# Kernel tuning notes

Measured on AMD Instinct MI355X. Metric: run time of the kernel, lower is better.

The kernel has to match this reference:

```python
import jax, jax.numpy as jnp
import numpy as np

D_MODEL = 1024
NUM_HEADS = 16
D_K = D_MODEL // NUM_HEADS


def setup_inputs() -> dict:
    key = jax.random.key(0)
    ks = jax.random.split(key, 8)
    B, S = 2, 2048
    query = jax.random.normal(ks[0], (B, S, D_MODEL), dtype=jnp.float32)
    k_in = jax.random.normal(ks[1], (B, S, D_MODEL), dtype=jnp.float32)
    value = jax.random.normal(ks[2], (B, S, D_MODEL), dtype=jnp.float32)
    # causal mask: True = masked out (upper triangle above diagonal)
    mask = jnp.triu(jnp.ones((S, S), dtype=bool), k=1)[None, None, :, :]
    scale = 1.0 / np.sqrt(D_MODEL)
    W_q = jax.random.normal(ks[3], (D_MODEL, D_MODEL), dtype=jnp.float32) * scale
    W_k = jax.random.normal(ks[4], (D_MODEL, D_MODEL), dtype=jnp.float32) * scale
    W_v = jax.random.normal(ks[5], (D_MODEL, D_MODEL), dtype=jnp.float32) * scale
    W_o = jax.random.normal(ks[6], (D_MODEL, D_MODEL), dtype=jnp.float32) * scale
    return {"query": query, "key": k_in, "value": value, "mask": mask,
            "W_q": W_q, "W_k": W_k, "W_v": W_v, "W_o": W_o}


def _split(x):
    # [B, S, d_model] -> [B, h, S, d_k]
    B, S, _ = x.shape
    return x.reshape(B, S, NUM_HEADS, D_K).transpose(0, 2, 1, 3)


def reference(query, key, value, mask, W_q, W_k, W_v, W_o):
    # torch nn.Linear(bias=False): y = x @ W.T
    Q = _split(query @ W_q.T)   # [B, h, Sq, d_k]
    K = _split(key @ W_k.T)     # [B, h, Sk, d_k]
    V = _split(value @ W_v.T)   # [B, h, Sk, d_k]
    scores = jnp.einsum('bhqd,bhkd->bhqk', Q, K) / jnp.sqrt(jnp.float32(D_K))
    scores = jnp.where(mask, -jnp.inf, scores)
    attn_w = jax.nn.softmax(scores, axis=-1)
    attn_w = jnp.nan_to_num(attn_w, nan=0.0)
    out = jnp.einsum('bhqk,bhkd->bhqd', attn_w, V)  # [B, h, Sq, d_k]
    B, _, Sq, _ = out.shape
    merged = out.transpose(0, 2, 1, 3).reshape(B, Sq, D_MODEL)
    return merged @ W_o.T
```

## Files before the change

### kernel.cpp

```cpp
#include <hip/hip_runtime.h>
#include <hip/hip_bf16.h>
#include <stdint.h>

typedef __attribute__((ext_vector_type(4))) float f32x4;
typedef __attribute__((ext_vector_type(8))) __bf16 bf16x8;
typedef __attribute__((ext_vector_type(4))) unsigned short us4;
typedef __attribute__((ext_vector_type(4))) short v4ss;

#define SEQ 2048
#define DMODEL 1024
#define NH 16
#define DK 64
#define MTOT 4096

__device__ __forceinline__ unsigned short f2bf(float x) {
  union { float f; unsigned int u; } v; v.f = x;
  unsigned int r = v.u + 0x7fffu + ((v.u >> 16) & 1u);
  return (unsigned short)(r >> 16);
}

__device__ __forceinline__ f32x4 mfma_bf16(bf16x8 a, bf16x8 b, f32x4 c) {
  return __builtin_amdgcn_mfma_f32_16x16x32_bf16(a, b, c, 0, 0, 0);
}

__device__ __forceinline__ f32x4 mfma_k16(us4 a, us4 b, f32x4 c) {
#if __has_builtin(__builtin_amdgcn_mfma_f32_16x16x16bf16_1k)
  return __builtin_amdgcn_mfma_f32_16x16x16bf16_1k(
      __builtin_bit_cast(v4ss, a), __builtin_bit_cast(v4ss, b), c, 0, 0, 0);
#else
  union U { bf16x8 v; us4 h[2]; } ua, ub;
  us4 z = {0, 0, 0, 0};
  ua.h[0] = a; ua.h[1] = z;
  ub.h[0] = b; ub.h[1] = z;
  return mfma_bf16(ua.v, ub.v, c);
#endif
}

__device__ __forceinline__ void gload16(const unsigned short* g, unsigned short* l) {
  __builtin_amdgcn_global_load_lds((__attribute__((address_space(1))) void*)g,
                                   (__attribute__((address_space(3))) void*)l,
                                   16, 0, 0);
}

__global__ void cvt_all(const float* __restrict__ s0, const float* __restrict__ s1,
                        const float* __restrict__ s2, const float* __restrict__ s3,
                        const float* __restrict__ s4, const float* __restrict__ s5,
                        const float* __restrict__ s6,
                        unsigned short* __restrict__ d0, unsigned short* __restrict__ d1,
                        unsigned short* __restrict__ d2, unsigned short* __restrict__ d3,
                        unsigned short* __restrict__ d4, unsigned short* __restrict__ d5,
                        unsigned short* __restrict__ d6) {
  const int y = blockIdx.y;
  const float* s = y == 0 ? s0 : y == 1 ? s1 : y == 2 ? s2 : y == 3 ? s3
                 : y == 4 ? s4 : y == 5 ? s5 : s6;
  unsigned short* d = y == 0 ? d0 : y == 1 ? d1 : y == 2 ? d2 : y == 3 ? d3
                    : y == 4 ? d4 : y == 5 ? d5 : d6;
  const int n4 = (y < 3) ? (MTOT * DMODEL / 4) : (DMODEL * DMODEL / 4);
  const int stride = gridDim.x * blockDim.x;
  for (int i = blockIdx.x * blockDim.x + threadIdx.x; i < n4; i += stride) {
    f32x4 v = reinterpret_cast<const f32x4*>(s)[i];
    us4 o;
    o.x = f2bf(v.x); o.y = f2bf(v.y); o.z = f2bf(v.z); o.w = f2bf(v.w);
    reinterpret_cast<us4*>(d)[i] = o;
  }
}

__global__ __launch_bounds__(256) void gemm_qkv(
    const unsigned short* __restrict__ xq, const unsigned short* __restrict__ xk,
    const unsigned short* __restrict__ xv, const unsigned short* __restrict__ bwq,
    const unsigned short* __restrict__ bwk, const unsigned short* __restrict__ bwv,
    unsigned short* __restrict__ Qh, unsigned short* __restrict__ Kh,
    unsigned short* __restrict__ Vt) {
  const int z = blockIdx.z;
  const unsigned short* A = z == 0 ? xq : (z == 1 ? xk : xv);
  const unsigned short* B = z == 0 ? bwq : (z == 1 ? bwk : bwv);
  unsigned short* out = z == 0 ? Qh : (z == 1 ? Kh : Vt);
  const float scale = z == 0 ? 0.18033688011112042f : 1.0f;

  __shared__ __align__(16) unsigned short lA[128 * 32];
  __shared__ __align__(16) unsigned short lB[128 * 32];
  const int tid = threadIdx.x;
  const int lane = tid & 63;
  const int wid = tid >> 6;
  const int l15 = lane & 15, l4 = lane >> 4;
  const int bm = blockIdx.x, bn = blockIdx.y;
  const int wr = wid >> 1, wc = wid & 1;

  f32x4 acc[4][4] = {};

  const int chunk0 = (wid * 2 + 0) * 64 + lane;
  const int chunk1 = (wid * 2 + 1) * 64 + lane;
  const unsigned short* gA0 = A + (size_t)(bm * 128 + (chunk0 >> 2)) * 1024 + (chunk0 & 3) * 8;
  const unsigned short* gA1 = A + (size_t)(bm * 128 + (chunk1 >> 2)) * 1024 + (chunk1 & 3) * 8;
  const unsigned short* gB0 = B + (size_t)(bn * 128 + (chunk0 >> 2)) * 1024 + (chunk0 & 3) * 8;
  const unsigned short* gB1 = B + (size_t)(bn * 128 + (chunk1 >> 2)) * 1024 + (chunk1 & 3) * 8;
  unsigned short* lA0 = lA + (wid * 2 + 0) * 512;
  unsigned short* lA1 = lA + (wid * 2 + 1) * 512;
  unsigned short* lB0 = lB + (wid * 2 + 0) * 512;
  unsigned short* lB1 = lB + (wid * 2 + 1) * 512;

  for (int kt = 0; kt < 1024; kt += 32) {
    __syncthreads();
    gload16(gA0 + kt, lA0);
    gload16(gA1 + kt, lA1);
    gload16(gB0 + kt, lB0);
    gload16(gB1 + kt, lB1);
    __syncthreads();
    bf16x8 af[4], bfr[4];
#pragma unroll
    for (int i = 0; i < 4; ++i)
      af[i] = *reinterpret_cast<const bf16x8*>(&lA[(wr * 64 + i * 16 + l15) * 32 + l4 * 8]);
#pragma unroll
    for (int j = 0; j < 4; ++j)
      bfr[j] = *reinterpret_cast<const bf16x8*>(&lB[(wc * 64 + j * 16 + l15) * 32 + l4 * 8]);
#pragma unroll
    for (int i = 0; i < 4; ++i)
#pragma unroll
      for (int j = 0; j < 4; ++j)
        acc[i][j] = mfma_bf16(af[i], bfr[j], acc[i][j]);
  }

  const int row0 = bm * 128 + wr * 64;
  const int col0 = bn * 128 + wc * 64;

  if (z < 2) {
#pragma unroll
    for (int i = 0; i < 4; ++i) {
#pragma unroll
      for (int j = 0; j < 4; ++j) {
        const int n = col0 + j * 16 + l15;
        const int h = n >> 6, dd = n & 63;
#pragma unroll
        for (int r = 0; r < 4; ++r) {
          const int m = row0 + i * 16 + l4 * 4 + r;
          const int b = m >> 11, s = m & 2047;
          out[(size_t)(b * NH + h) * (SEQ * DK) + s * DK + dd] = f2bf(acc[i][j][r] * scale);
        }
      }
    }
  } else {
#pragma unroll
    for (int i = 0; i < 4; ++i) {
      const int m0 = row0 + i * 16 + l4 * 4;
      const int b = m0 >> 11, s0 = m0 & 2047;
#pragma unroll
      for (int j = 0; j < 4; ++j) {
        const int n = col0 + j * 16 + l15;
        const int h = n >> 6, dd = n & 63;
        us4 pk;
        pk.x = f2bf(acc[i][j][0]);
        pk.y = f2bf(acc[i][j][1]);
        pk.z = f2bf(acc[i][j][2]);
        pk.w = f2bf(acc[i][j][3]);
        *reinterpret_cast<us4*>(&out[(size_t)(b * NH + h) * (DK * SEQ) + dd * SEQ + s0]) = pk;
      }
    }
  }
}

__global__ __launch_bounds__(256) void gemm_o(const unsigned short* __restrict__ A,
                                              const unsigned short* __restrict__ B,
                                              float* __restrict__ out) {
  __shared__ __align__(16) unsigned short lA[128 * 32];
  __shared__ __align__(16) unsigned short lB[128 * 32];
  const int tid = threadIdx.x;
  const int lane = tid & 63;
  const int wid = tid >> 6;
  const int l15 = lane & 15, l4 = lane >> 4;
  const int bm = blockIdx.x, bn = blockIdx.y;
  const int wr = wid >> 1, wc = wid & 1;

  f32x4 acc[4][4] = {};

  const int chunk0 = (wid * 2 + 0) * 64 + lane;
  const int chunk1 = (wid * 2 + 1) * 64 + lane;
  const unsigned short* gA0 = A + (size_t)(bm * 128 + (chunk0 >> 2)) * 1024 + (chunk0 & 3) * 8;
  const unsigned short* gA1 = A + (size_t)(bm * 128 + (chunk1 >> 2)) * 1024 + (chunk1 & 3) * 8;
  const unsigned short* gB0 = B + (size_t)(bn * 128 + (chunk0 >> 2)) * 1024 + (chunk0 & 3) * 8;
  const unsigned short* gB1 = B + (size_t)(bn * 128 + (chunk1 >> 2)) * 1024 + (chunk1 & 3) * 8;
  unsigned short* lA0 = lA + (wid * 2 + 0) * 512;
  unsigned short* lA1 = lA + (wid * 2 + 1) * 512;
  unsigned short* lB0 = lB + (wid * 2 + 0) * 512;
  unsigned short* lB1 = lB + (wid * 2 + 1) * 512;

  for (int kt = 0; kt < 1024; kt += 32) {
    __syncthreads();
    gload16(gA0 + kt, lA0);
    gload16(gA1 + kt, lA1);
    gload16(gB0 + kt, lB0);
    gload16(gB1 + kt, lB1);
    __syncthreads();
    bf16x8 af[4], bfr[4];
#pragma unroll
    for (int i = 0; i < 4; ++i)
      af[i] = *reinterpret_cast<const bf16x8*>(&lA[(wr * 64 + i * 16 + l15) * 32 + l4 * 8]);
#pragma unroll
    for (int j = 0; j < 4; ++j)
      bfr[j] = *reinterpret_cast<const bf16x8*>(&lB[(wc * 64 + j * 16 + l15) * 32 + l4 * 8]);
#pragma unroll
    for (int i = 0; i < 4; ++i)
#pragma unroll
      for (int j = 0; j < 4; ++j)
        acc[i][j] = mfma_bf16(af[i], bfr[j], acc[i][j]);
  }

  const int row0 = bm * 128 + wr * 64;
  const int col0 = bn * 128 + wc * 64;
#pragma unroll
  for (int i = 0; i < 4; ++i)
#pragma unroll
    for (int j = 0; j < 4; ++j)
#pragma unroll
      for (int r = 0; r < 4; ++r) {
        const int m = row0 + i * 16 + l4 * 4 + r;
        const int n = col0 + j * 16 + l15;
        out[(size_t)m * DMODEL + n] = acc[i][j][r];
      }
}

__global__ __launch_bounds__(512, 2) void attn_kernel(const unsigned short* __restrict__ Qh,
                                                      const unsigned short* __restrict__ Kh,
                                                      const unsigned short* __restrict__ Vt,
                                                      unsigned short* __restrict__ Mg) {
  __shared__ __align__(16) unsigned short Kl[3][64 * 64];
  __shared__ __align__(16) unsigned short Vl[3][64 * 64];

  const int tid = threadIdx.x;
  const int lane = tid & 63;
  const int w = tid >> 6;
  const int l15 = lane & 15, l4 = lane >> 4;

  const int d = blockIdx.x;
  const int xcd = d & 7;
  const int j = d >> 3;
  const int bh = (j >> 3) * 8 + xcd;
  const int x = j & 7;

  const unsigned short* Qb = Qh + (size_t)bh * SEQ * DK;
  const unsigned short* Kb = Kh + (size_t)bh * SEQ * DK;
  const unsigned short* Vb = Vt + (size_t)bh * DK * SEQ;
  const int bq = bh >> 4, hh = bh & 15;
  unsigned short* Mbase = Mg + (size_t)bq * SEQ * DMODEL + hh * DK;

  const int srow = lane >> 3;
  const int sswz = (lane & 7) ^ srow;
  const unsigned short* KsrcB = Kb + (size_t)(w * 8 + srow) * DK + sswz * 8;
  const unsigned short* VsrcB = Vb + (size_t)(w * 8 + srow) * SEQ + sswz * 8;

  const int l7 = l15 & 7;

  const int taus[2] = {15 - x, x};

#pragma unroll 1
  for (int seg = 0; seg < 2; ++seg) {
    const int tau = taus[seg];
    const int qbase = tau * 128;
    const int q0w = qbase + w * 16;
    const int nt = 2 * tau + 2;

    __syncthreads();

    bf16x8 qf0 = *reinterpret_cast<const bf16x8*>(Qb + (size_t)(q0w + l15) * DK + l4 * 8);
    bf16x8 qf1 = *reinterpret_cast<const bf16x8*>(Qb + (size_t)(q0w + l15) * DK + 32 + l4 * 8);

    f32x4 o[4] = {};
    float mrow = -__builtin_inff();
    float lrow = 0.0f;

    gload16(KsrcB, &Kl[0][w * 512]);
    gload16(VsrcB, &Vl[0][w * 512]);
    gload16(KsrcB + (size_t)64 * DK, &Kl[1][w * 512]);
    gload16(VsrcB + 64, &Vl[1][w * 512]);

    int bi = 0;
#pragma unroll 1
    for (int t = 0; t < nt; ++t) {
      const int kbase = t << 6;
      if (t + 1 < nt) {
        asm volatile("s_waitcnt vmcnt(2)" ::: "memory");
      } else {
        asm volatile("s_waitcnt vmcnt(0)" ::: "memory");
      }
      __builtin_amdgcn_sched_barrier(0);
      __builtin_amdgcn_s_barrier();
      __builtin_amdgcn_sched_barrier(0);

      if (t + 2 < nt) {
        const int pb = (bi == 0) ? 2 : bi - 1;
        gload16(KsrcB + (size_t)(kbase + 128) * DK, &Kl[pb][w * 512]);
        gload16(VsrcB + (kbase + 128), &Vl[pb][w * 512]);
      }

      if (kbase < q0w + 16) {
        const unsigned short* Kc = Kl[bi];
        const unsigned short* Vc = Vl[bi];

        f32x4 sc[4];
#pragma unroll
        for (int c = 0; c < 4; ++c) {
          const int krow = c * 16 + l15;
          bf16x8 kf0 = *reinterpret_cast<const bf16x8*>(&Kc[krow * 64 + ((l4 ^ l7) * 8)]);
          bf16x8 kf1 = *reinterpret_cast<const bf16x8*>(&Kc[krow * 64 + (((4 + l4) ^ l7) * 8)]);
          f32x4 z = {0.f, 0.f, 0.f, 0.f};
          z = mfma_bf16(kf0, qf0, z);
          sc[c] = mfma_bf16(kf1, qf1, z);
        }

        if (kbase + 63 > q0w) {
          const int qg = q0w + l15;
#pragma unroll
          for (int c = 0; c < 4; ++c) {
            const int kp = kbase + c * 16 + l4 * 4;
#pragma unroll
            for (int r = 0; r < 4; ++r)
              if (kp + r > qg) sc[c][r] = -__builtin_inff();
          }
        }

        f32x4 mv = sc[0];
#pragma unroll
        for (int c = 1; c < 4; ++c)
#pragma unroll
          for (int r = 0; r < 4; ++r) mv[r] = fmaxf(mv[r], sc[c][r]);
        float pm = fmaxf(fmaxf(mv[0], mv[1]), fmaxf(mv[2], mv[3]));
        pm = fmaxf(pm, __shfl_xor(pm, 16));
        pm = fmaxf(pm, __shfl_xor(pm, 32));
        const float mn = fmaxf(mrow, pm);
        const float al = __builtin_amdgcn_exp2f(mrow - mn);
        mrow = mn;
        f32x4 sv = {0.f, 0.f, 0.f, 0.f};
        us4 pb4[4];
#pragma unroll
        for (int c = 0; c < 4; ++c) {
#pragma unroll
          for (int r = 0; r < 4; ++r) {
            const float p = __builtin_amdgcn_exp2f(sc[c][r] - mn);
            sc[c][r] = p;
            sv[r] += p;
          }
          us4 pk;
          pk.x = f2bf(sc[c][0]);
          pk.y = f2bf(sc[c][1]);
          pk.z = f2bf(sc[c][2]);
          pk.w = f2bf(sc[c][3]);
          pb4[c] = pk;
        }
        float rs = (sv[0] + sv[1]) + (sv[2] + sv[3]);
        rs += __shfl_xor(rs, 16);
        rs += __shfl_xor(rs, 32);
        lrow = lrow * al + rs;
#pragma unroll
        for (int dd = 0; dd < 4; ++dd)
#pragma unroll
          for (int r = 0; r < 4; ++r) o[dd][r] *= al;

#pragma unroll
        for (int dd = 0; dd < 4; ++dd) {
          const int vrow = dd * 16 + l15;
#pragma unroll
          for (int c = 0; c < 4; ++c) {
            const us4 va = *reinterpret_cast<const us4*>(
                &Vc[vrow * 64 + (((c * 2 + (l4 >> 1)) ^ l7) * 8) + (l4 & 1) * 4]);
            o[dd] = mfma_k16(va, pb4[c], o[dd]);
          }
        }
      }

      bi = (bi == 2) ? 0 : bi + 1;
    }

    const float inv = __builtin_amdgcn_rcpf(lrow);
    const int s = q0w + l15;
#pragma unroll
    for (int dd = 0; dd < 4; ++dd) {
      us4 pk;
      pk.x = f2bf(o[dd][0] * inv);
      pk.y = f2bf(o[dd][1] * inv);
      pk.z = f2bf(o[dd][2] * inv);
      pk.w = f2bf(o[dd][3] * inv);
      *reinterpret_cast<us4*>(&Mbase[(size_t)s * DMODEL + dd * 16 + l4 * 4]) = pk;
    }
  }
}

extern "C" void kernel_launch(void* const* d_in, const int* in_sizes, int n_in,
                              void* d_out, int out_size, void* d_ws, size_t ws_size,
                              hipStream_t stream) {
  (void)in_sizes; (void)n_in; (void)out_size;
  if (ws_size < (size_t)64 * (1 << 20)) return;

  const float* q = (const float*)d_in[0];
  const float* k = (const float*)d_in[1];
  const float* v = (const float*)d_in[2];
  const float* wq = (const float*)d_in[4];
  const float* wk = (const float*)d_in[5];
  const float* wv = (const float*)d_in[6];
  const float* wo = (const float*)d_in[7];

  char* ws = (char*)d_ws;
  unsigned short* xq  = (unsigned short*)(ws + (size_t)0  * (1 << 20));
  unsigned short* xk  = (unsigned short*)(ws + (size_t)8  * (1 << 20));
  unsigned short* xv  = (unsigned short*)(ws + (size_t)16 * (1 << 20));
  unsigned short* bwq = (unsigned short*)(ws + (size_t)24 * (1 << 20));
  unsigned short* bwk = (unsigned short*)(ws + (size_t)26 * (1 << 20));
  unsigned short* bwv = (unsigned short*)(ws + (size_t)28 * (1 << 20));
  unsigned short* bwo = (unsigned short*)(ws + (size_t)30 * (1 << 20));
  unsigned short* Qh  = (unsigned short*)(ws + (size_t)32 * (1 << 20));
  unsigned short* Kh  = (unsigned short*)(ws + (size_t)40 * (1 << 20));
  unsigned short* Vt  = (unsigned short*)(ws + (size_t)48 * (1 << 20));
  unsigned short* Mg  = (unsigned short*)(ws + (size_t)56 * (1 << 20));

  cvt_all<<<dim3(256, 7), 256, 0, stream>>>(q, k, v, wq, wk, wv, wo,
                                            xq, xk, xv, bwq, bwk, bwv, bwo);
  gemm_qkv<<<dim3(32, 8, 3), 256, 0, stream>>>(xq, xk, xv, bwq, bwk, bwv, Qh, Kh, Vt);
  attn_kernel<<<dim3(256), 512, 0, stream>>>(Qh, Kh, Vt, Mg);
  gemm_o<<<dim3(32, 8), 256, 0, stream>>>(Mg, bwo, (float*)d_out);
}
```

Measured before the change: 145.2 us.

## Use lazy softmax rescaling, K32 PV MFMA with permuted V layout, packed bf16 converts

The attention inner loop skips the online-softmax max reduction and output rescale unless some row's max grows by more than a threshold, and defers the row-sum shuffle reduction to the end. The V transpose store is permuted so that PV can use the 16x16x32 bf16 MFMA with 8-wide fragments instead of four 16x16x16 MFMAs. Probabilities and outputs are packed with the hardware v_cvt_pk_bf16_f32 instruction, and s_setprio raises wave priority around the MFMA blocks. These cut VALU, shuffle and MFMA issue cost, at the risk of larger exponent values when the lazy threshold allows a stale max.

```diff
diff --git a/kernel.cpp b/kernel.cpp
--- a/kernel.cpp
+++ b/kernel.cpp
@@ -5,7 +5,6 @@
 typedef __attribute__((ext_vector_type(4))) float f32x4;
 typedef __attribute__((ext_vector_type(8))) __bf16 bf16x8;
 typedef __attribute__((ext_vector_type(4))) unsigned short us4;
-typedef __attribute__((ext_vector_type(4))) short v4ss;
 
 #define SEQ 2048
 #define DMODEL 1024
@@ -19,21 +18,14 @@
   return (unsigned short)(r >> 16);
 }
 
+__device__ __forceinline__ unsigned int cvtpk(float lo, float hi) {
+  unsigned int r;
+  asm("v_cvt_pk_bf16_f32 %0, %1, %2" : "=v"(r) : "v"(lo), "v"(hi));
+  return r;
+}
+
 __device__ __forceinline__ f32x4 mfma_bf16(bf16x8 a, bf16x8 b, f32x4 c) {
   return __builtin_amdgcn_mfma_f32_16x16x32_bf16(a, b, c, 0, 0, 0);
-}
-
-__device__ __forceinline__ f32x4 mfma_k16(us4 a, us4 b, f32x4 c) {
-#if __has_builtin(__builtin_amdgcn_mfma_f32_16x16x16bf16_1k)
-  return __builtin_amdgcn_mfma_f32_16x16x16bf16_1k(
-      __builtin_bit_cast(v4ss, a), __builtin_bit_cast(v4ss, b), c, 0, 0, 0);
-#else
-  union U { bf16x8 v; us4 h[2]; } ua, ub;
-  us4 z = {0, 0, 0, 0};
-  ua.h[0] = a; ua.h[1] = z;
-  ub.h[0] = b; ub.h[1] = z;
-  return mfma_bf16(ua.v, ub.v, c);
-#endif
 }
 
 __device__ __forceinline__ void gload16(const unsigned short* g, unsigned short* l) {
@@ -143,6 +135,8 @@
     for (int i = 0; i < 4; ++i) {
       const int m0 = row0 + i * 16 + l4 * 4;
       const int b = m0 >> 11, s0 = m0 & 2047;
+      const int g = (s0 >> 2) & 7;
+      const int col = (s0 & ~31) + ((g & 3) << 3) + ((g >> 2) << 2);
 #pragma unroll
       for (int j = 0; j < 4; ++j) {
         const int n = col0 + j * 16 + l15;
@@ -152,7 +146,7 @@
         pk.y = f2bf(acc[i][j][1]);
         pk.z = f2bf(acc[i][j][2]);
         pk.w = f2bf(acc[i][j][3]);
-        *reinterpret_cast<us4*>(&out[(size_t)(b * NH + h) * (DK * SEQ) + dd * SEQ + s0]) = pk;
+        *reinterpret_cast<us4*>(&out[(size_t)(b * NH + h) * (DK * SEQ) + dd * SEQ + col]) = pk;
       }
     }
   }
@@ -296,6 +290,7 @@
         const unsigned short* Vc = Vl[bi];
 
         f32x4 sc[4];
+        __builtin_amdgcn_s_setprio(1);
 #pragma unroll
         for (int c = 0; c < 4; ++c) {
           const int krow = c * 16 + l15;
@@ -305,6 +300,7 @@
           z = mfma_bf16(kf0, qf0, z);
           sc[c] = mfma_bf16(kf1, qf1, z);
         }
+        __builtin_amdgcn_s_setprio(0);
 
         if (kbase + 63 > q0w) {
           const int qg = q0w + l15;
@@ -323,62 +319,59 @@
 #pragma unroll
           for (int r = 0; r < 4; ++r) mv[r] = fmaxf(mv[r], sc[c][r]);
         float pm = fmaxf(fmaxf(mv[0], mv[1]), fmaxf(mv[2], mv[3]));
-        pm = fmaxf(pm, __shfl_xor(pm, 16));
-        pm = fmaxf(pm, __shfl_xor(pm, 32));
-        const float mn = fmaxf(mrow, pm);
-        const float al = __builtin_amdgcn_exp2f(mrow - mn);
-        mrow = mn;
+        if (!__all(pm - mrow <= 8.0f)) {
+          pm = fmaxf(pm, __shfl_xor(pm, 16));
+          pm = fmaxf(pm, __shfl_xor(pm, 32));
+          const float mn = fmaxf(mrow, pm);
+          const float al = __builtin_amdgcn_exp2f(mrow - mn);
+          mrow = mn;
+          lrow *= al;
+#pragma unroll
+          for (int dd = 0; dd < 4; ++dd)
+#pragma unroll
+            for (int r = 0; r < 4; ++r) o[dd][r] *= al;
+        }
+        union PB { bf16x8 v; unsigned int u[4]; } pbv[2];
         f32x4 sv = {0.f, 0.f, 0.f, 0.f};
-        us4 pb4[4];
 #pragma unroll
         for (int c = 0; c < 4; ++c) {
-#pragma unroll
-          for (int r = 0; r < 4; ++r) {
-            const float p = __builtin_amdgcn_exp2f(sc[c][r] - mn);
-            sc[c][r] = p;
-            sv[r] += p;
-          }
-          us4 pk;
-          pk.x = f2bf(sc[c][0]);
-          pk.y = f2bf(sc[c][1]);
-          pk.z = f2bf(sc[c][2]);
-          pk.w = f2bf(sc[c][3]);
-          pb4[c] = pk;
-        }
-        float rs = (sv[0] + sv[1]) + (sv[2] + sv[3]);
-        rs += __shfl_xor(rs, 16);
-        rs += __shfl_xor(rs, 32);
-        lrow = lrow * al + rs;
-#pragma unroll
-        for (int dd = 0; dd < 4; ++dd)
-#pragma unroll
-          for (int r = 0; r < 4; ++r) o[dd][r] *= al;
-
+          const float p0 = __builtin_amdgcn_exp2f(sc[c][0] - mrow);
+          const float p1 = __builtin_amdgcn_exp2f(sc[c][1] - mrow);
+          const float p2 = __builtin_amdgcn_exp2f(sc[c][2] - mrow);
+          const float p3 = __builtin_amdgcn_exp2f(sc[c][3] - mrow);
+          sv[0] += p0; sv[1] += p1; sv[2] += p2; sv[3] += p3;
+          pbv[c >> 1].u[(c & 1) * 2 + 0] = cvtpk(p0, p1);
+          pbv[c >> 1].u[(c & 1) * 2 + 1] = cvtpk(p2, p3);
+        }
+        lrow += (sv[0] + sv[1]) + (sv[2] + sv[3]);
+
+        __builtin_amdgcn_s_setprio(1);
 #pragma unroll
         for (int dd = 0; dd < 4; ++dd) {
           const int vrow = dd * 16 + l15;
 #pragma unroll
-          for (int c = 0; c < 4; ++c) {
-            const us4 va = *reinterpret_cast<const us4*>(
-                &Vc[vrow * 64 + (((c * 2 + (l4 >> 1)) ^ l7) * 8) + (l4 & 1) * 4]);
-            o[dd] = mfma_k16(va, pb4[c], o[dd]);
+          for (int p = 0; p < 2; ++p) {
+            const bf16x8 av = *reinterpret_cast<const bf16x8*>(
+                &Vc[vrow * 64 + (((p * 4 + l4) ^ l7) * 8)]);
+            o[dd] = mfma_bf16(av, pbv[p].v, o[dd]);
           }
         }
+        __builtin_amdgcn_s_setprio(0);
       }
 
       bi = (bi == 2) ? 0 : bi + 1;
     }
 
+    lrow += __shfl_xor(lrow, 16);
+    lrow += __shfl_xor(lrow, 32);
     const float inv = __builtin_amdgcn_rcpf(lrow);
     const int s = q0w + l15;
 #pragma unroll
     for (int dd = 0; dd < 4; ++dd) {
-      us4 pk;
-      pk.x = f2bf(o[dd][0] * inv);
-      pk.y = f2bf(o[dd][1] * inv);
-      pk.z = f2bf(o[dd][2] * inv);
-      pk.w = f2bf(o[dd][3] * inv);
-      *reinterpret_cast<us4*>(&Mbase[(size_t)s * DMODEL + dd * 16 + l4 * 4]) = pk;
+      union { us4 h; unsigned int u[2]; } pk;
+      pk.u[0] = cvtpk(o[dd][0] * inv, o[dd][1] * inv);
+      pk.u[1] = cvtpk(o[dd][2] * inv, o[dd][3] * inv);
+      *reinterpret_cast<us4*>(&Mbase[(size_t)s * DMODEL + dd * 16 + l4 * 4]) = pk.h;
     }
   }
 }
```

Result: faster. 135.7 us (-6.5%).
